# Kernel tuning notes

Measured on AMD Instinct MI355X. Metric: run time of the kernel, lower is better.

Reference implementation:

```python
import jax, jax.numpy as jnp
import numpy as np

K = 4
G = 64
IN_DIM = 256
OUT_DIM = 256
BATCH = 512
T0, T1 = -1.0, 1.0


def setup_inputs() -> dict:
    key = jax.random.key(0)
    kx, kw = jax.random.split(key)
    x = jax.random.uniform(kx, (BATCH, IN_DIM), jnp.float32, T0, T1)
    # xavier_normal_ on [G+K, in, out]: std = sqrt(2 / (fan_in + fan_out)) with fan over last two dims
    std = (2.0 / (IN_DIM + OUT_DIM)) ** 0.5
    w = jax.random.normal(kw, (G + K, IN_DIM, OUT_DIM), jnp.float32) * std
    # knot vector: k-1 repeats of t0, linspace(t0,t1,G+1), k-1 repeats of t1
    t = jnp.concatenate([
        jnp.full((K - 1,), T0, jnp.float32),
        jnp.linspace(T0, T1, G + 1, dtype=jnp.float32),
        jnp.full((K - 1,), T1, jnp.float32),
    ])
    return {"x": x, "w": w, "t": t, "k": K}


def _basis(x, t, k):
    """Cox-de Boor: the k nonzero order-k B-spline basis values at each x.
    Returns (idx, N): idx [..., k] basis indices i-k+1..i, N [..., k] values."""
    n_t = t.shape[0]
    # interval i with t[i] <= x < t[i+1], clipped to the valid span
    i = jnp.clip(jnp.searchsorted(t, x, side='right') - 1, k - 1, n_t - k - 1)
    N = jnp.ones(x.shape + (1,), x.dtype)
    for p in range(1, k):  # static small loop (k=4)
        jj = jnp.arange(1, p + 1)
        left = x[..., None] - t[i[..., None] + 1 - jj]   # [..., p]
        right = t[i[..., None] + jj] - x[..., None]      # [..., p]
        saved = jnp.zeros_like(x)
        vals = []
        for r in range(p):
            d = right[..., r] + left[..., p - 1 - r]      # t[i+r+1] - t[i+r+1-p]
            temp = N[..., r] / d
            vals.append(saved + right[..., r] * temp)
            saved = left[..., p - 1 - r] * temp
        vals.append(saved)
        N = jnp.stack(vals, -1)
    idx = i[..., None] - (k - 1) + jnp.arange(k)
    return idx, N


def reference(x, w, t, k):
    in_dim = x.shape[1]
    n_rows = w.shape[0]
    idx, y1 = _basis(x, t, k)                             # [B,in,k], [B,in,k]
    # last row of w (index -1 == n_rows-1) weights the SiLU residual term
    idx_full = jnp.concatenate(
        [idx, jnp.full(idx.shape[:-1] + (1,), n_rows - 1, idx.dtype)], -1)  # [B,in,k+1]
    silu = x * jax.nn.sigmoid(x)
    y2 = jnp.concatenate([y1, silu[..., None]], -1)       # [B,in,k+1]
    # gather local spline coefficients: w2[b,c,j,o] = w[idx_full[b,c,j], c, o]
    w2 = w[idx_full, jnp.arange(in_dim)[None, :, None], :]  # [B,in,k+1,out]
    return jnp.einsum('bcjo,bcj->bo', w2, y2)             # [B,out]
```

## Files before the change

kernel.cpp:

```cpp
#include <hip/hip_runtime.h>
#include <math.h>
#include <stdint.h>

#define IN_DIM  256
#define OUT_DIM 256
#define NROWS   68
#define NT      71
#define BATCH   512
#define W_ELEMS (NROWS * IN_DIM * OUT_DIM)
#define PART_FLOATS (4 * BATCH * OUT_DIM)

__device__ __forceinline__ uint32_t bf16_rne(float f) {
  uint32_t u = __builtin_bit_cast(uint32_t, f);
  return (u + 0x7fffu + ((u >> 16) & 1u)) >> 16;
}

__global__ __launch_bounds__(256) void cvt_kernel(const float* __restrict__ w,
                                                  uint32_t* __restrict__ wb) {
  const int base = (blockIdx.x * 256 + threadIdx.x) * 8;
  const float4 a = *(const float4*)(w + base);
  const float4 b = *(const float4*)(w + base + 4);
  uint4 o;
  o.x = bf16_rne(a.x) | (bf16_rne(a.y) << 16);
  o.y = bf16_rne(a.z) | (bf16_rne(a.w) << 16);
  o.z = bf16_rne(b.x) | (bf16_rne(b.y) << 16);
  o.w = bf16_rne(b.z) | (bf16_rne(b.w) << 16);
  *(uint4*)(wb + base / 2) = o;
}

__device__ __forceinline__ void fma8(const uint4 q, const float y, float* acc) {
  acc[0] += y * __builtin_bit_cast(float, q.x << 16);
  acc[1] += y * __builtin_bit_cast(float, q.x & 0xffff0000u);
  acc[2] += y * __builtin_bit_cast(float, q.y << 16);
  acc[3] += y * __builtin_bit_cast(float, q.y & 0xffff0000u);
  acc[4] += y * __builtin_bit_cast(float, q.z << 16);
  acc[5] += y * __builtin_bit_cast(float, q.z & 0xffff0000u);
  acc[6] += y * __builtin_bit_cast(float, q.w << 16);
  acc[7] += y * __builtin_bit_cast(float, q.w & 0xffff0000u);
}

__global__ __launch_bounds__(256) void kan_gather_kernel(
    const float* __restrict__ x, const uint4* __restrict__ wp,
    const float* __restrict__ t, float* __restrict__ part) {
  __shared__ float  lt[NT];
  __shared__ float4 lyv[64];
  __shared__ float  lys[64];
  __shared__ int    lbase[64];
  __shared__ float  red[8 * 32 * 9];

  const int tid = threadIdx.x;
  const unsigned bid = blockIdx.x;
  const int sl = (bid & 7) >> 1;
  const int b  = ((bid & 1) << 8) | (bid >> 3);

  if (tid < NT) lt[tid] = t[tid];
  __syncthreads();

  if (tid < 64) {
    const int c = sl * 64 + tid;
    const float xv = x[b * IN_DIM + c];
    int i = 3 + (int)floorf((xv + 1.0f) * 32.0f);
    i = i < 3 ? 3 : (i > 66 ? 66 : i);
    while (i > 3 && xv < lt[i]) --i;
    while (i < 66 && xv >= lt[i + 1]) ++i;

    float N0 = 1.f, N1 = 0.f, N2 = 0.f, N3 = 0.f;
    {
      const float l1 = xv - lt[i];
      const float r1 = lt[i + 1] - xv;
      const float tp = N0 / (r1 + l1);
      N1 = l1 * tp; N0 = r1 * tp;
    }
    {
      const float l1 = xv - lt[i];
      const float l2 = xv - lt[i - 1];
      const float r1 = lt[i + 1] - xv;
      const float r2 = lt[i + 2] - xv;
      float saved = 0.f;
      const float tp0 = N0 / (r1 + l2);
      const float n0 = saved + r1 * tp0; saved = l2 * tp0;
      const float tp1 = N1 / (r2 + l1);
      const float n1 = saved + r2 * tp1; saved = l1 * tp1;
      N0 = n0; N1 = n1; N2 = saved;
    }
    {
      const float l1 = xv - lt[i];
      const float l2 = xv - lt[i - 1];
      const float l3 = xv - lt[i - 2];
      const float r1 = lt[i + 1] - xv;
      const float r2 = lt[i + 2] - xv;
      const float r3 = lt[i + 3] - xv;
      float saved = 0.f;
      const float tp0 = N0 / (r1 + l3);
      const float n0 = saved + r1 * tp0; saved = l3 * tp0;
      const float tp1 = N1 / (r2 + l2);
      const float n1 = saved + r2 * tp1; saved = l2 * tp1;
      const float tp2 = N2 / (r3 + l1);
      const float n2 = saved + r3 * tp2; saved = l1 * tp2;
      N0 = n0; N1 = n1; N2 = n2; N3 = saved;
    }
    lyv[tid]   = make_float4(N0, N1, N2, N3);
    lys[tid]   = xv / (1.0f + expf(-xv));
    lbase[tid] = i - 3;
  }
  __syncthreads();

  const int ol = tid & 31;
  const int cs = tid >> 5;

  float acc[8] = {0.f, 0.f, 0.f, 0.f, 0.f, 0.f, 0.f, 0.f};
  const int cbeg = cs * 8;
  #pragma unroll 2
  for (int m = 0; m < 8; ++m) {
    const int cl = cbeg + m;
    const float4 yv = lyv[cl];
    const float  ys = lys[cl];
    const int base  = lbase[cl];
    const uint4* p  = wp + (size_t)(sl * 64 + cl) * 32 + ol;
    const uint4 q0 = p[(size_t)(base + 0) * 8192];
    const uint4 q1 = p[(size_t)(base + 1) * 8192];
    const uint4 q2 = p[(size_t)(base + 2) * 8192];
    const uint4 q3 = p[(size_t)(base + 3) * 8192];
    const uint4 q4 = p[(size_t)67 * 8192];
    fma8(q0, yv.x, acc);
    fma8(q1, yv.y, acc);
    fma8(q2, yv.z, acc);
    fma8(q3, yv.w, acc);
    fma8(q4, ys,   acc);
  }

  float* r = &red[(cs * 32 + ol) * 9];
  #pragma unroll
  for (int j = 0; j < 8; ++j) r[j] = acc[j];
  __syncthreads();
  if (tid < 64) {
    const int olr = tid >> 1;
    const int jb  = (tid & 1) * 4;
    float4 s = make_float4(0.f, 0.f, 0.f, 0.f);
    #pragma unroll
    for (int sI = 0; sI < 8; ++sI) {
      const float* rr = &red[(sI * 32 + olr) * 9 + jb];
      s.x += rr[0]; s.y += rr[1]; s.z += rr[2]; s.w += rr[3];
    }
    ((float4*)(part + ((size_t)sl * BATCH + b) * OUT_DIM))[tid] = s;
  }
}

__global__ __launch_bounds__(256) void reduce_kernel(const float* __restrict__ part,
                                                     float* __restrict__ out) {
  const int q = blockIdx.x * 256 + threadIdx.x;
  const float4* p0 = (const float4*)(part);
  const float4* p1 = (const float4*)(part + BATCH * OUT_DIM);
  const float4* p2 = (const float4*)(part + 2 * BATCH * OUT_DIM);
  const float4* p3 = (const float4*)(part + 3 * BATCH * OUT_DIM);
  const float4 a = p0[q], b = p1[q], c = p2[q], d = p3[q];
  float4 s;
  s.x = (a.x + b.x) + (c.x + d.x);
  s.y = (a.y + b.y) + (c.y + d.y);
  s.z = (a.z + b.z) + (c.z + d.z);
  s.w = (a.w + b.w) + (c.w + d.w);
  ((float4*)out)[q] = s;
}

extern "C" void kernel_launch(void* const* d_in, const int* in_sizes, int n_in,
                              void* d_out, int out_size, void* d_ws, size_t ws_size,
                              hipStream_t stream) {
  const float* x = (const float*)d_in[0];
  const float* w = (const float*)d_in[1];
  const float* t = (const float*)d_in[2];
  float* out  = (float*)d_out;
  float* part = (float*)d_ws;
  uint32_t* wb = (uint32_t*)d_ws + PART_FLOATS;
  cvt_kernel<<<W_ELEMS / (256 * 8), 256, 0, stream>>>(w, wb);
  kan_gather_kernel<<<BATCH * 4, 256, 0, stream>>>(x, (const uint4*)wb, t, part);
  reduce_kernel<<<BATCH * OUT_DIM / 4 / 256, 256, 0, stream>>>(part, out);
}
```

Measured before the change: 90.49 us.

## Split SiLU residual into a dense GEMM fused with partial reduction

The SiLU residual term uses the same weight row for every input, so it is pulled out of the gather kernel and computed as a small dense tiled GEMM (silu(x) times w[67]). That GEMM kernel also sums the four partial slices, replacing the separate reduce kernel. The gather loop is manually software-pipelined with explicit issue/consume macros, now loading four rows per channel instead of five, and declares an occupancy hint of eight blocks per SM. The risk is that the new GEMM runs on only 32 blocks, which may underuse the GPU and sit on the critical path.

```diff
diff --git a/kernel.cpp b/kernel.cpp
--- a/kernel.cpp
+++ b/kernel.cpp
@@ -39,12 +39,23 @@
   acc[7] += y * __builtin_bit_cast(float, q.w & 0xffff0000u);
 }
 
-__global__ __launch_bounds__(256) void kan_gather_kernel(
+#define ISSUE(n, cl)                                        \
+  const int rb##n = ((sl * 64 + (cl)) * 32 + ol) + lbase[cl] * 8192; \
+  const uint4 q##n##0 = wp[rb##n];                          \
+  const uint4 q##n##1 = wp[rb##n + 8192];                   \
+  const uint4 q##n##2 = wp[rb##n + 16384];                  \
+  const uint4 q##n##3 = wp[rb##n + 24576];
+
+#define CONSUME(n, cl) {                                    \
+  const float4 yv = lyv[cl];                                \
+  fma8(q##n##0, yv.x, acc); fma8(q##n##1, yv.y, acc);       \
+  fma8(q##n##2, yv.z, acc); fma8(q##n##3, yv.w, acc); }
+
+__global__ __launch_bounds__(256, 8) void kan_gather_kernel(
     const float* __restrict__ x, const uint4* __restrict__ wp,
     const float* __restrict__ t, float* __restrict__ part) {
   __shared__ float  lt[NT];
   __shared__ float4 lyv[64];
-  __shared__ float  lys[64];
   __shared__ int    lbase[64];
   __shared__ float  red[8 * 32 * 9];
 
@@ -100,33 +111,32 @@
       N0 = n0; N1 = n1; N2 = n2; N3 = saved;
     }
     lyv[tid]   = make_float4(N0, N1, N2, N3);
-    lys[tid]   = xv / (1.0f + expf(-xv));
     lbase[tid] = i - 3;
   }
   __syncthreads();
 
   const int ol = tid & 31;
   const int cs = tid >> 5;
+  const int cbeg = cs * 8;
 
   float acc[8] = {0.f, 0.f, 0.f, 0.f, 0.f, 0.f, 0.f, 0.f};
-  const int cbeg = cs * 8;
-  #pragma unroll 2
-  for (int m = 0; m < 8; ++m) {
-    const int cl = cbeg + m;
-    const float4 yv = lyv[cl];
-    const float  ys = lys[cl];
-    const int base  = lbase[cl];
-    const uint4* p  = wp + (size_t)(sl * 64 + cl) * 32 + ol;
-    const uint4 q0 = p[(size_t)(base + 0) * 8192];
-    const uint4 q1 = p[(size_t)(base + 1) * 8192];
-    const uint4 q2 = p[(size_t)(base + 2) * 8192];
-    const uint4 q3 = p[(size_t)(base + 3) * 8192];
-    const uint4 q4 = p[(size_t)67 * 8192];
-    fma8(q0, yv.x, acc);
-    fma8(q1, yv.y, acc);
-    fma8(q2, yv.z, acc);
-    fma8(q3, yv.w, acc);
-    fma8(q4, ys,   acc);
+  {
+    ISSUE(0, cbeg + 0)
+    ISSUE(1, cbeg + 1)
+    CONSUME(0, cbeg + 0)
+    ISSUE(2, cbeg + 2)
+    CONSUME(1, cbeg + 1)
+    ISSUE(3, cbeg + 3)
+    CONSUME(2, cbeg + 2)
+    ISSUE(4, cbeg + 4)
+    CONSUME(3, cbeg + 3)
+    ISSUE(5, cbeg + 5)
+    CONSUME(4, cbeg + 4)
+    ISSUE(6, cbeg + 6)
+    CONSUME(5, cbeg + 5)
+    ISSUE(7, cbeg + 7)
+    CONSUME(6, cbeg + 6)
+    CONSUME(7, cbeg + 7)
   }
 
   float* r = &red[(cs * 32 + ol) * 9];
@@ -146,20 +156,77 @@
   }
 }
 
-__global__ __launch_bounds__(256) void reduce_kernel(const float* __restrict__ part,
-                                                     float* __restrict__ out) {
-  const int q = blockIdx.x * 256 + threadIdx.x;
-  const float4* p0 = (const float4*)(part);
-  const float4* p1 = (const float4*)(part + BATCH * OUT_DIM);
-  const float4* p2 = (const float4*)(part + 2 * BATCH * OUT_DIM);
-  const float4* p3 = (const float4*)(part + 3 * BATCH * OUT_DIM);
-  const float4 a = p0[q], b = p1[q], c = p2[q], d = p3[q];
-  float4 s;
-  s.x = (a.x + b.x) + (c.x + d.x);
-  s.y = (a.y + b.y) + (c.y + d.y);
-  s.z = (a.z + b.z) + (c.z + d.z);
-  s.w = (a.w + b.w) + (c.w + d.w);
-  ((float4*)out)[q] = s;
+__device__ __forceinline__ float bflo(uint32_t u) {
+  return __builtin_bit_cast(float, u << 16);
+}
+__device__ __forceinline__ float bfhi(uint32_t u) {
+  return __builtin_bit_cast(float, u & 0xffff0000u);
+}
+
+__global__ __launch_bounds__(256) void silu_out_kernel(
+    const float* __restrict__ x, const uint32_t* __restrict__ wb,
+    const float* __restrict__ part, float* __restrict__ out) {
+  __shared__ float AsT[32][68];
+  __shared__ float Bs[32][68];
+
+  const int tid = threadIdx.x;
+  const int bx = blockIdx.x & 3;
+  const int by = blockIdx.x >> 2;
+  const int b0 = by * 64, o0 = bx * 64;
+  const int tb = tid >> 4;
+  const int to = tid & 15;
+
+  float acc[4][4] = {};
+  const uint32_t* w67 = wb + 67 * 32768 + bx * 32;
+
+  for (int kk = 0; kk < 8; ++kk) {
+    __syncthreads();
+    {
+      const int row  = tid >> 3;
+      const int kcol = (tid & 7) * 4;
+      #pragma unroll
+      for (int e = 0; e < 2; ++e) {
+        const int rr = row + e * 32;
+        const float4 v = *(const float4*)(x + (b0 + rr) * IN_DIM + kk * 32 + kcol);
+        AsT[kcol + 0][rr] = v.x / (1.f + expf(-v.x));
+        AsT[kcol + 1][rr] = v.y / (1.f + expf(-v.y));
+        AsT[kcol + 2][rr] = v.z / (1.f + expf(-v.z));
+        AsT[kcol + 3][rr] = v.w / (1.f + expf(-v.w));
+      }
+    }
+    {
+      const int k  = tid >> 3;
+      const int up = (tid & 7) * 4;
+      const uint4 q = *(const uint4*)(w67 + (kk * 32 + k) * 128 + up);
+      float* br = &Bs[k][up * 2];
+      float4 f0 = make_float4(bflo(q.x), bfhi(q.x), bflo(q.y), bfhi(q.y));
+      float4 f1 = make_float4(bflo(q.z), bfhi(q.z), bflo(q.w), bfhi(q.w));
+      *(float4*)(br + 0) = f0;
+      *(float4*)(br + 4) = f1;
+    }
+    __syncthreads();
+    #pragma unroll
+    for (int k = 0; k < 32; ++k) {
+      const float4 a  = *(const float4*)&AsT[k][tb * 4];
+      const float4 bq = *(const float4*)&Bs[k][to * 4];
+      acc[0][0] += a.x * bq.x; acc[0][1] += a.x * bq.y; acc[0][2] += a.x * bq.z; acc[0][3] += a.x * bq.w;
+      acc[1][0] += a.y * bq.x; acc[1][1] += a.y * bq.y; acc[1][2] += a.y * bq.z; acc[1][3] += a.y * bq.w;
+      acc[2][0] += a.z * bq.x; acc[2][1] += a.z * bq.y; acc[2][2] += a.z * bq.z; acc[2][3] += a.z * bq.w;
+      acc[3][0] += a.w * bq.x; acc[3][1] += a.w * bq.y; acc[3][2] += a.w * bq.z; acc[3][3] += a.w * bq.w;
+    }
+  }
+
+  #pragma unroll
+  for (int i = 0; i < 4; ++i) {
+    const int b = b0 + tb * 4 + i;
+    float4 r = make_float4(acc[i][0], acc[i][1], acc[i][2], acc[i][3]);
+    #pragma unroll
+    for (int sI = 0; sI < 4; ++sI) {
+      const float4 p = *(const float4*)(part + ((size_t)(sI * BATCH + b)) * OUT_DIM + o0 + to * 4);
+      r.x += p.x; r.y += p.y; r.z += p.z; r.w += p.w;
+    }
+    *(float4*)(out + (size_t)b * OUT_DIM + o0 + to * 4) = r;
+  }
 }
 
 extern "C" void kernel_launch(void* const* d_in, const int* in_sizes, int n_in,
@@ -173,5 +240,5 @@
   uint32_t* wb = (uint32_t*)d_ws + PART_FLOATS;
   cvt_kernel<<<W_ELEMS / (256 * 8), 256, 0, stream>>>(w, wb);
   kan_gather_kernel<<<BATCH * 4, 256, 0, stream>>>(x, (const uint4*)wb, t, part);
-  reduce_kernel<<<BATCH * OUT_DIM / 4 / 256, 256, 0, stream>>>(part, out);
-}
+  silu_out_kernel<<<32, 256, 0, stream>>>(x, wb, part, out);
+}
```

New measurement: 184.9 us. 104% more time.

## Move SiLU residual term out of gather kernel into fused final reduce kernel

Applied to the files above, without the earlier changes.

Drops the SiLU basis term (row 67 of the weights) from the per-batch, per-input-slice gather loop. It is now computed in a new per-batch kernel that does a dense 256x256 matvec against row 67 and also sums the four partial slices, replacing the separate reduce kernel. The gather loop loses one of its five weight loads per input column, and the small reduce pass is absorbed into the new kernel. In exchange the new kernel has 512 blocks, each re-reading the full row-67 weight slice, which should mostly hit cache.

```diff
diff --git a/kernel.cpp b/kernel.cpp
--- a/kernel.cpp
+++ b/kernel.cpp
@@ -44,7 +44,6 @@
     const float* __restrict__ t, float* __restrict__ part) {
   __shared__ float  lt[NT];
   __shared__ float4 lyv[64];
-  __shared__ float  lys[64];
   __shared__ int    lbase[64];
   __shared__ float  red[8 * 32 * 9];
 
@@ -100,7 +99,6 @@
       N0 = n0; N1 = n1; N2 = n2; N3 = saved;
     }
     lyv[tid]   = make_float4(N0, N1, N2, N3);
-    lys[tid]   = xv / (1.0f + expf(-xv));
     lbase[tid] = i - 3;
   }
   __syncthreads();
@@ -114,19 +112,16 @@
   for (int m = 0; m < 8; ++m) {
     const int cl = cbeg + m;
     const float4 yv = lyv[cl];
-    const float  ys = lys[cl];
     const int base  = lbase[cl];
     const uint4* p  = wp + (size_t)(sl * 64 + cl) * 32 + ol;
     const uint4 q0 = p[(size_t)(base + 0) * 8192];
     const uint4 q1 = p[(size_t)(base + 1) * 8192];
     const uint4 q2 = p[(size_t)(base + 2) * 8192];
     const uint4 q3 = p[(size_t)(base + 3) * 8192];
-    const uint4 q4 = p[(size_t)67 * 8192];
     fma8(q0, yv.x, acc);
     fma8(q1, yv.y, acc);
     fma8(q2, yv.z, acc);
     fma8(q3, yv.w, acc);
-    fma8(q4, ys,   acc);
   }
 
   float* r = &red[(cs * 32 + ol) * 9];
@@ -146,20 +141,55 @@
   }
 }
 
-__global__ __launch_bounds__(256) void reduce_kernel(const float* __restrict__ part,
-                                                     float* __restrict__ out) {
-  const int q = blockIdx.x * 256 + threadIdx.x;
-  const float4* p0 = (const float4*)(part);
-  const float4* p1 = (const float4*)(part + BATCH * OUT_DIM);
-  const float4* p2 = (const float4*)(part + 2 * BATCH * OUT_DIM);
-  const float4* p3 = (const float4*)(part + 3 * BATCH * OUT_DIM);
-  const float4 a = p0[q], b = p1[q], c = p2[q], d = p3[q];
-  float4 s;
-  s.x = (a.x + b.x) + (c.x + d.x);
-  s.y = (a.y + b.y) + (c.y + d.y);
-  s.z = (a.z + b.z) + (c.z + d.z);
-  s.w = (a.w + b.w) + (c.w + d.w);
-  ((float4*)out)[q] = s;
+__global__ __launch_bounds__(256) void silu_out_kernel(
+    const float* __restrict__ x, const uint32_t* __restrict__ wb,
+    const float* __restrict__ part, float* __restrict__ out) {
+  __shared__ float sx[IN_DIM];
+  __shared__ float red[8 * 32 * 9];
+
+  const int tid = threadIdx.x;
+  const int b   = blockIdx.x;
+
+  {
+    const float xv = x[b * IN_DIM + tid];
+    sx[tid] = xv / (1.f + expf(-xv));
+  }
+  __syncthreads();
+
+  const int ol = tid & 31;
+  const int ks = tid >> 5;
+  const uint4* __restrict__ w67 = (const uint4*)(wb + 67 * 32768);
+
+  float acc[8] = {0.f, 0.f, 0.f, 0.f, 0.f, 0.f, 0.f, 0.f};
+  const int kbeg = ks * 32;
+  #pragma unroll 4
+  for (int m = 0; m < 32; ++m) {
+    const int k = kbeg + m;
+    const uint4 q = w67[k * 32 + ol];
+    fma8(q, sx[k], acc);
+  }
+
+  float* r = &red[(ks * 32 + ol) * 9];
+  #pragma unroll
+  for (int j = 0; j < 8; ++j) r[j] = acc[j];
+  __syncthreads();
+  if (tid < 64) {
+    const int olr = tid >> 1;
+    const int jb  = (tid & 1) * 4;
+    float4 s = make_float4(0.f, 0.f, 0.f, 0.f);
+    #pragma unroll
+    for (int sI = 0; sI < 8; ++sI) {
+      const float* rr = &red[(sI * 32 + olr) * 9 + jb];
+      s.x += rr[0]; s.y += rr[1]; s.z += rr[2]; s.w += rr[3];
+    }
+    const int off = olr * 8 + jb;
+    #pragma unroll
+    for (int sI = 0; sI < 4; ++sI) {
+      const float4 p = *(const float4*)(part + ((size_t)sI * BATCH + b) * OUT_DIM + off);
+      s.x += p.x; s.y += p.y; s.z += p.z; s.w += p.w;
+    }
+    *(float4*)(out + (size_t)b * OUT_DIM + off) = s;
+  }
 }
 
 extern "C" void kernel_launch(void* const* d_in, const int* in_sizes, int n_in,
@@ -173,5 +203,5 @@
   uint32_t* wb = (uint32_t*)d_ws + PART_FLOATS;
   cvt_kernel<<<W_ELEMS / (256 * 8), 256, 0, stream>>>(w, wb);
   kan_gather_kernel<<<BATCH * 4, 256, 0, stream>>>(x, (const uint4*)wb, t, part);
-  reduce_kernel<<<BATCH * OUT_DIM / 4 / 256, 256, 0, stream>>>(part, out);
-}
+  silu_out_kernel<<<BATCH, 256, 0, stream>>>(x, wb, part, out);
+}
```

After: 92.07 us. No clear change (+1.7%).
